# Performance work log

Hardware: AMD Instinct MI355X
Metric: run time of the kernel (lower is better)

The kernel has to match this reference:

```python
import jax, jax.numpy as jnp
import numpy as np

B, C, H, W = 4, 256, 64, 64
RED = 8
DQK = C // RED  # 32


def setup_inputs() -> dict:
    key = jax.random.key(0)
    ks = jax.random.split(key, 8)
    x = jax.random.normal(ks[0], (B, C, H, W), dtype=jnp.float32)
    # 1x1 conv weights == per-pixel linear maps: [out_ch, in_ch] + bias [out_ch]
    q_w = jax.random.normal(ks[1], (DQK, C), dtype=jnp.float32) * (1.0 / np.sqrt(C))
    q_b = jax.random.normal(ks[2], (DQK,), dtype=jnp.float32) * 0.01
    k_w = jax.random.normal(ks[3], (DQK, C), dtype=jnp.float32) * (1.0 / np.sqrt(C))
    k_b = jax.random.normal(ks[4], (DQK,), dtype=jnp.float32) * 0.01
    v_w = jax.random.normal(ks[5], (C, C), dtype=jnp.float32) * (1.0 / np.sqrt(C))
    v_b = jax.random.normal(ks[6], (C,), dtype=jnp.float32) * 0.01
    # gamma is init'd to 0 in torch; use a nonzero value so the attention path matters
    gamma = jax.random.normal(ks[7], (1,), dtype=jnp.float32) * 0.1
    return {"x": x, "q_w": q_w, "q_b": q_b, "k_w": k_w, "k_b": k_b,
            "v_w": v_w, "v_b": v_b, "gamma": gamma}


def reference(x, q_w, q_b, k_w, k_b, v_w, v_b, gamma):
    b, c, h, w = x.shape
    xf = x.reshape(b, c, h * w)  # [B, C, N]
    # 1x1 convs as channel matmuls
    q = jnp.einsum('dc,bcn->bdn', q_w, xf) + q_b[None, :, None]  # [B, DQK, N]
    k = jnp.einsum('dc,bcn->bdn', k_w, xf) + k_b[None, :, None]  # [B, DQK, N]
    v = jnp.einsum('oc,bcn->bon', v_w, xf) + v_b[None, :, None]  # [B, C, N]
    # attn[b, n, m] = softmax_m( q[:,n] . k[:,m] )  -- NO 1/sqrt(d) scale (faithful)
    scores = jnp.einsum('bdn,bdm->bnm', q, k)  # [B, N, N]
    attn = jax.nn.softmax(scores, axis=-1)
    # out = v @ attn^T : out[b, c, n] = sum_m v[b, c, m] * attn[b, n, m]
    out = jnp.einsum('bcm,bnm->bcn', v, attn).reshape(b, c, h, w)
    return gamma[0] * out + x
```

## Files before the change

kernel.cpp:

```cpp
#include <hip/hip_runtime.h>

#define NN 4096
#define CC 256
#define DQ 32

typedef __attribute__((ext_vector_type(8))) short short8;
typedef __attribute__((ext_vector_type(4))) float f32x4;

__device__ __forceinline__ unsigned short f32_to_bf16(float f) {
  unsigned int u = __float_as_uint(f);
  u += 0x7fffu + ((u >> 16) & 1u);
  return (unsigned short)(u >> 16);
}

__device__ __forceinline__ float exp2_hw(float f) {
  return __builtin_amdgcn_exp2f(f);
}

__device__ __forceinline__ unsigned cvt_pk_bf16(float lo, float hi) {
  unsigned r;
  asm("v_cvt_pk_bf16_f32 %0, %1, %2" : "=v"(r) : "v"(lo), "v"(hi));
  return r;
}

__device__ __forceinline__ void gld16(const void* g, void* l) {
  __builtin_amdgcn_global_load_lds(
      (__attribute__((address_space(1))) void*)(g),
      (__attribute__((address_space(3))) void*)(l), 16, 0, 0);
}

__global__ __launch_bounds__(256) void wconv_kernel(
    const float* qw, const float* kw, const float* vw,
    const float* qb, const float* kb, const float* vb,
    unsigned short* Wcat, float* bcat) {
  int id = blockIdx.x * 256 + threadIdx.x;
  if (id < 320 * 256) {
    int row = id >> 8;
    float v;
    if (row < 32) v = qw[id];
    else if (row < 64) v = kw[id - 32 * 256];
    else v = vw[id - 64 * 256];
    Wcat[id] = f32_to_bf16(v);
  }
  if (id < 320) {
    float v;
    if (id < 32) v = qb[id];
    else if (id < 64) v = kb[id - 32];
    else v = vb[id - 64];
    bcat[id] = v;
  }
}

__global__ __launch_bounds__(256) void proj_kernel(
    const float* x, const unsigned short* Wcat, const float* bcat,
    unsigned short* Qt, unsigned short* Kt, unsigned short* V) {
  int bid = blockIdx.x;
  int b = bid >> 6, nb = bid & 63;
  int tid = threadIdx.x, lane = tid & 63, w = tid >> 6;
  int l15 = lane & 15, h = lane >> 4;
  int n0 = nb * 64 + w * 16;

  __shared__ unsigned short xT[64][264];
  {
    const float* xb = x + ((size_t)b * CC) * NN + nb * 64;
    int c0 = tid >> 4, n4 = (tid & 15) * 4;
#pragma unroll
    for (int i = 0; i < 16; i++) {
      int c = c0 + i * 16;
      f32x4 v = *(const f32x4*)(xb + (size_t)c * NN + n4);
#pragma unroll
      for (int j = 0; j < 4; j++) xT[n4 + j][c] = f32_to_bf16(v[j]);
    }
  }
  __syncthreads();

  int nl = w * 16 + l15;
  short8 af[8];
#pragma unroll
  for (int ks = 0; ks < 8; ks++)
    af[ks] = *(const short8*)(&xT[nl][ks * 32 + h * 8]);

  f32x4 acc[20];
#pragma unroll
  for (int t = 0; t < 20; t++)
#pragma unroll
    for (int r = 0; r < 4; r++) acc[t][r] = 0.f;

#pragma unroll
  for (int ks = 0; ks < 8; ks++) {
#pragma unroll
    for (int dt = 0; dt < 20; dt++) {
      short8 bfr = *(const short8*)(Wcat + (size_t)(dt * 16 + l15) * CC + ks * 32 + h * 8);
      acc[dt] = __builtin_amdgcn_mfma_f32_16x16x32_bf16(af[ks], bfr, acc[dt], 0, 0, 0);
    }
  }

  unsigned short* Qtb = Qt + (size_t)b * NN * DQ;
  unsigned short* Ktb = Kt + (size_t)b * NN * DQ;
#pragma unroll
  for (int dt = 0; dt < 4; dt++) {
    float bias = bcat[dt * 16 + l15];
    float scale = dt < 2 ? 1.44269504f : 1.0f;
    unsigned short* dst = dt < 2 ? Qtb : Ktb;
    int dd = (dt & 1) * 16 + l15;
#pragma unroll
    for (int r = 0; r < 4; r++) {
      int n = n0 + h * 4 + r;
      dst[(size_t)n * DQ + dd] = f32_to_bf16((acc[dt][r] + bias) * scale);
    }
  }

  __shared__ unsigned short vbuf[CC][64];
  __syncthreads();
#pragma unroll
  for (int dt = 4; dt < 20; dt++) {
    float bias = bcat[dt * 16 + l15];
    int c = (dt - 4) * 16 + l15;
#pragma unroll
    for (int r = 0; r < 4; r++) {
      int nl2 = w * 16 + h * 4 + r;
      vbuf[c][nl2] = f32_to_bf16(acc[dt][r] + bias);
    }
  }
  __syncthreads();
  unsigned short* Vb = V + (size_t)b * CC * NN + nb * 64;
  for (int cc = 0; cc < 64; cc++) {
    int c = w * 64 + cc;
    Vb[(size_t)c * NN + lane] = vbuf[c][lane];
  }
}

__global__ __launch_bounds__(512) void attn_kernel(
    const unsigned short* Qt, const unsigned short* Kt, const unsigned short* V,
    const float* x, const float* gamma, float* out) {
  int bid = blockIdx.x;
  int b = (bid & 7) >> 1;
  int nb = (bid >> 3) * 2 + (bid & 1);
  int tid = threadIdx.x, lane = tid & 63, w = tid >> 6;
  int grp = w >> 2;
  int wq = w & 3;
  int wc = w & 3;
  int l15 = lane & 15, h = lane >> 4;
  int n0 = nb * 64 + wq * 16;

  const unsigned short* Qtb = Qt + (size_t)b * NN * DQ;
  const unsigned short* Ktb = Kt + (size_t)b * NN * DQ;
  const unsigned short* Vb  = V  + (size_t)b * CC * NN;

  __shared__ __align__(16) unsigned short vbuf[4][CC * 64];
  __shared__ __align__(16) unsigned short pbuf[8][16 * 64];
  __shared__ float sstat[8][16];

  short8 qf = *(const short8*)(Qtb + (size_t)(n0 + l15) * DQ + h * 8);

  f32x4 acc[16];
#pragma unroll
  for (int t = 0; t < 16; t++)
#pragma unroll
    for (int r = 0; r < 4; r++) acc[t][r] = 0.f;
  float rs = 0.f;

  f32x4 zero4;
#pragma unroll
  for (int r = 0; r < 4; r++) zero4[r] = 0.f;

  auto stageSS = [&](int t) {
#pragma unroll
    for (int ch = 0; ch < 2; ch++) {
      int ck = 2 * t + ch;
      int m0 = ck * 64;
      char* dst = (char*)&vbuf[ck & 3][0];
#pragma unroll
      for (int it = 0; it < 4; it++) {
        int idx = it * 512 + tid;
        int c = idx >> 3, sub = idx & 7;
        int moff = (sub ^ (c & 7)) * 8;
        gld16(Vb + (size_t)c * NN + m0 + moff, dst + idx * 16);
      }
    }
  };

#define KLOAD(T, KF) do { int ci_ = 2 * (T) + grp; \
  _Pragma("unroll") for (int s_ = 0; s_ < 4; s_++) \
    KF[s_] = *(const short8*)(Ktb + (size_t)(ci_ * 64 + s_ * 16 + l15) * DQ + h * 8); \
} while (0)

  short8 kA[4], kB[4];
  stageSS(0);
  KLOAD(0, kA);

#define SUPERSTEP(T, KF, KN) do { \
  __syncthreads();   \
  if ((T) + 1 < 32) stageSS((T) + 1); \
  f32x4 st[4]; \
  _Pragma("unroll") for (int s = 0; s < 4; s++) \
    st[s] = __builtin_amdgcn_mfma_f32_16x16x32_bf16(KF[s], qf, zero4, 0, 0, 0); \
  if ((T) + 1 < 32) KLOAD((T) + 1, KN); \
  float lsum = 0.f; \
  unsigned p32[8]; \
  _Pragma("unroll") for (int s = 0; s < 4; s++) { \
    float e0 = exp2_hw(st[s][0]); \
    float e1 = exp2_hw(st[s][1]); \
    float e2 = exp2_hw(st[s][2]); \
    float e3 = exp2_hw(st[s][3]); \
    lsum += (e0 + e1) + (e2 + e3); \
    p32[s * 2 + 0] = cvt_pk_bf16(e0, e1); \
    p32[s * 2 + 1] = cvt_pk_bf16(e2, e3); \
  } \
  rs += lsum; \
  { char* pb = (char*)&pbuf[w][0]; \
  _Pragma("unroll") for (int s = 0; s < 4; s++) { \
    int2 pv; pv.x = (int)p32[s * 2]; pv.y = (int)p32[s * 2 + 1]; \
    int inner = (s * 32 + h * 8) ^ ((l15 & 7) << 4); \
    *(int2*)(pb + l15 * 128 + inner) = pv; \
  } } \
   \
  asm volatile("s_waitcnt lgkmcnt(0)" ::: "memory"); \
  __builtin_amdgcn_s_barrier(); \
  asm volatile("" ::: "memory"); \
  { const char* vb2 = (const char*)&vbuf[(2 * (T) + grp) & 3][0]; \
  __builtin_amdgcn_s_setprio(1); \
  _Pragma("unroll") for (int p = 0; p < 2; p++) { \
    int pinner = (p * 64 + h * 16) ^ ((l15 & 7) << 4); \
    short8 pf0 = *(const short8*)((const char*)&pbuf[grp * 4 + 0][0] + l15 * 128 + pinner); \
    short8 pf1 = *(const short8*)((const char*)&pbuf[grp * 4 + 1][0] + l15 * 128 + pinner); \
    short8 pf2 = *(const short8*)((const char*)&pbuf[grp * 4 + 2][0] + l15 * 128 + pinner); \
    short8 pf3 = *(const short8*)((const char*)&pbuf[grp * 4 + 3][0] + l15 * 128 + pinner); \
    _Pragma("unroll") for (int ct = 0; ct < 4; ct++) { \
      int c = wc * 64 + ct * 16 + l15; \
      int sub = (p * 4 + h) ^ (c & 7); \
      short8 vf = *(const short8*)(vb2 + c * 128 + sub * 16); \
      acc[ct * 4 + 0] = __builtin_amdgcn_mfma_f32_16x16x32_bf16(vf, pf0, acc[ct * 4 + 0], 0, 0, 0); \
      acc[ct * 4 + 1] = __builtin_amdgcn_mfma_f32_16x16x32_bf16(vf, pf1, acc[ct * 4 + 1], 0, 0, 0); \
      acc[ct * 4 + 2] = __builtin_amdgcn_mfma_f32_16x16x32_bf16(vf, pf2, acc[ct * 4 + 2], 0, 0, 0); \
      acc[ct * 4 + 3] = __builtin_amdgcn_mfma_f32_16x16x32_bf16(vf, pf3, acc[ct * 4 + 3], 0, 0, 0); \
    } \
  } \
  __builtin_amdgcn_s_setprio(0); } \
} while (0)

  for (int t2 = 0; t2 < 16; t2++) {
    SUPERSTEP(2 * t2, kA, kB);
    SUPERSTEP(2 * t2 + 1, kB, kA);
  }
#undef SUPERSTEP
#undef KLOAD

  rs += __shfl_xor(rs, 16);
  rs += __shfl_xor(rs, 32);
  if (h == 0) sstat[w][l15] = rs;
  __syncthreads();

  float* sacc = (float*)&vbuf[0][0];
  if (grp == 1) {
#pragma unroll
    for (int ct = 0; ct < 4; ct++)
#pragma unroll
      for (int nt = 0; nt < 4; nt++)
        *(f32x4*)(sacc + ((wc * 16 + ct * 4 + nt) << 8) + lane * 4) = acc[ct * 4 + nt];
  }
  __syncthreads();

  if (grp == 0) {
    float g = gamma[0];
    float invv[4];
#pragma unroll
    for (int nt = 0; nt < 4; nt++)
      invv[nt] = 1.0f / (sstat[nt][l15] + sstat[4 + nt][l15]);
    const float* xb = x + (size_t)b * CC * NN;
    float* ob = out + (size_t)b * CC * NN;
#pragma unroll
    for (int ct = 0; ct < 4; ct++)
#pragma unroll
      for (int nt = 0; nt < 4; nt++) {
        f32x4 ap = *(const f32x4*)(sacc + ((wc * 16 + ct * 4 + nt) << 8) + lane * 4);
#pragma unroll
        for (int r = 0; r < 4; r++) {
          int c = wc * 64 + ct * 16 + h * 4 + r;
          size_t off = (size_t)c * NN + (size_t)nb * 64 + nt * 16 + l15;
          ob[off] = g * (acc[ct * 4 + nt][r] + ap[r]) * invv[nt] + xb[off];
        }
      }
  }
}

extern "C" void kernel_launch(void* const* d_in, const int* in_sizes, int n_in,
                              void* d_out, int out_size, void* d_ws, size_t ws_size,
                              hipStream_t stream) {
  (void)in_sizes; (void)n_in; (void)out_size; (void)ws_size;
  const float* x  = (const float*)d_in[0];
  const float* qw = (const float*)d_in[1];
  const float* qb = (const float*)d_in[2];
  const float* kw = (const float*)d_in[3];
  const float* kb = (const float*)d_in[4];
  const float* vw = (const float*)d_in[5];
  const float* vb = (const float*)d_in[6];
  const float* gamma = (const float*)d_in[7];
  float* out = (float*)d_out;

  char* ws = (char*)d_ws;
  unsigned short* Wcat = (unsigned short*)(ws);
  float*          bcat = (float*)(ws + 163840);
  unsigned short* Qt   = (unsigned short*)(ws + 165120);
  unsigned short* Kt   = (unsigned short*)(ws + 1213696);
  unsigned short* V    = (unsigned short*)(ws + 2262272);

  hipLaunchKernelGGL(wconv_kernel, dim3(320), dim3(256), 0, stream,
                     qw, kw, vw, qb, kb, vb, Wcat, bcat);
  hipLaunchKernelGGL(proj_kernel, dim3(256), dim3(256), 0, stream,
                     x, Wcat, bcat, Qt, Kt, V);
  hipLaunchKernelGGL(attn_kernel, dim3(256), dim3(512), 0, stream,
                     Qt, Kt, V, x, gamma, out);
}
```

Before: 105.0 us.

## Split attention over key halves with 1024-thread blocks and separate fuse kernel

The attention kernel now gives each block 128 query rows and half of the key range, using 16 waves per block. It writes bf16 partial outputs and row sums to workspace, and a new fuse kernel combines the two halves with the residual. The projection kernel also moves to 32-pixel tiles across 512 blocks, with vectorized V stores. The aim is more parallelism and wider query reuse of each staged V tile, at the cost of an extra launch, extra partial-buffer traffic and bf16 rounding of the partial sums.

```diff
diff --git a/kernel.cpp b/kernel.cpp
--- a/kernel.cpp
+++ b/kernel.cpp
@@ -11,6 +11,10 @@
   unsigned int u = __float_as_uint(f);
   u += 0x7fffu + ((u >> 16) & 1u);
   return (unsigned short)(u >> 16);
+}
+
+__device__ __forceinline__ float bf16_to_f32(unsigned short u) {
+  return __uint_as_float(((unsigned int)u) << 16);
 }
 
 __device__ __forceinline__ float exp2_hw(float f) {
@@ -55,18 +59,18 @@
     const float* x, const unsigned short* Wcat, const float* bcat,
     unsigned short* Qt, unsigned short* Kt, unsigned short* V) {
   int bid = blockIdx.x;
-  int b = bid >> 6, nb = bid & 63;
+  int b = bid >> 7, nb = bid & 127;
   int tid = threadIdx.x, lane = tid & 63, w = tid >> 6;
   int l15 = lane & 15, h = lane >> 4;
-  int n0 = nb * 64 + w * 16;
-
-  __shared__ unsigned short xT[64][264];
+
+  __shared__ unsigned short xT[32][272];
+  __shared__ unsigned short vbuf[CC][32];
   {
-    const float* xb = x + ((size_t)b * CC) * NN + nb * 64;
-    int c0 = tid >> 4, n4 = (tid & 15) * 4;
-#pragma unroll
-    for (int i = 0; i < 16; i++) {
-      int c = c0 + i * 16;
+    const float* xb = x + (size_t)b * CC * NN + nb * 32;
+    int c0 = tid >> 3, n4 = (tid & 7) * 4;
+#pragma unroll
+    for (int i = 0; i < 8; i++) {
+      int c = c0 + i * 32;
       f32x4 v = *(const f32x4*)(xb + (size_t)c * NN + n4);
 #pragma unroll
       for (int j = 0; j < 4; j++) xT[n4 + j][c] = f32_to_bf16(v[j]);
@@ -74,82 +78,76 @@
   }
   __syncthreads();
 
-  int nl = w * 16 + l15;
+  int ntile = w & 1, dt0 = (w >> 1) * 10;
   short8 af[8];
 #pragma unroll
   for (int ks = 0; ks < 8; ks++)
-    af[ks] = *(const short8*)(&xT[nl][ks * 32 + h * 8]);
-
-  f32x4 acc[20];
-#pragma unroll
-  for (int t = 0; t < 20; t++)
+    af[ks] = *(const short8*)(&xT[ntile * 16 + l15][ks * 32 + h * 8]);
+
+  f32x4 acc[10];
+#pragma unroll
+  for (int t = 0; t < 10; t++)
 #pragma unroll
     for (int r = 0; r < 4; r++) acc[t][r] = 0.f;
 
 #pragma unroll
   for (int ks = 0; ks < 8; ks++) {
 #pragma unroll
-    for (int dt = 0; dt < 20; dt++) {
+    for (int d = 0; d < 10; d++) {
+      int dt = dt0 + d;
       short8 bfr = *(const short8*)(Wcat + (size_t)(dt * 16 + l15) * CC + ks * 32 + h * 8);
-      acc[dt] = __builtin_amdgcn_mfma_f32_16x16x32_bf16(af[ks], bfr, acc[dt], 0, 0, 0);
+      acc[d] = __builtin_amdgcn_mfma_f32_16x16x32_bf16(af[ks], bfr, acc[d], 0, 0, 0);
     }
   }
 
   unsigned short* Qtb = Qt + (size_t)b * NN * DQ;
   unsigned short* Ktb = Kt + (size_t)b * NN * DQ;
 #pragma unroll
-  for (int dt = 0; dt < 4; dt++) {
+  for (int d = 0; d < 10; d++) {
+    int dt = dt0 + d;
     float bias = bcat[dt * 16 + l15];
-    float scale = dt < 2 ? 1.44269504f : 1.0f;
-    unsigned short* dst = dt < 2 ? Qtb : Ktb;
-    int dd = (dt & 1) * 16 + l15;
-#pragma unroll
-    for (int r = 0; r < 4; r++) {
-      int n = n0 + h * 4 + r;
-      dst[(size_t)n * DQ + dd] = f32_to_bf16((acc[dt][r] + bias) * scale);
-    }
-  }
-
-  __shared__ unsigned short vbuf[CC][64];
+    if (dt < 4) {
+      float scale = dt < 2 ? 1.44269504f : 1.0f;
+      unsigned short* dst = dt < 2 ? Qtb : Ktb;
+      int dd = (dt & 1) * 16 + l15;
+#pragma unroll
+      for (int r = 0; r < 4; r++) {
+        int n = nb * 32 + ntile * 16 + h * 4 + r;
+        dst[(size_t)n * DQ + dd] = f32_to_bf16((acc[d][r] + bias) * scale);
+      }
+    } else {
+      int c = (dt - 4) * 16 + l15;
+#pragma unroll
+      for (int r = 0; r < 4; r++)
+        vbuf[c][ntile * 16 + h * 4 + r] = f32_to_bf16(acc[d][r] + bias);
+    }
+  }
   __syncthreads();
-#pragma unroll
-  for (int dt = 4; dt < 20; dt++) {
-    float bias = bcat[dt * 16 + l15];
-    int c = (dt - 4) * 16 + l15;
-#pragma unroll
-    for (int r = 0; r < 4; r++) {
-      int nl2 = w * 16 + h * 4 + r;
-      vbuf[c][nl2] = f32_to_bf16(acc[dt][r] + bias);
-    }
-  }
-  __syncthreads();
-  unsigned short* Vb = V + (size_t)b * CC * NN + nb * 64;
-  for (int cc = 0; cc < 64; cc++) {
-    int c = w * 64 + cc;
-    Vb[(size_t)c * NN + lane] = vbuf[c][lane];
-  }
-}
-
-__global__ __launch_bounds__(512) void attn_kernel(
+  unsigned short* Vb = V + (size_t)b * CC * NN + nb * 32;
+  int c = tid;
+#pragma unroll
+  for (int k = 0; k < 4; k++)
+    *(f32x4*)(Vb + (size_t)c * NN + k * 8) = *(const f32x4*)(&vbuf[c][k * 8]);
+}
+
+__global__ __launch_bounds__(1024) void attn_kernel(
     const unsigned short* Qt, const unsigned short* Kt, const unsigned short* V,
-    const float* x, const float* gamma, float* out) {
+    unsigned short* Apart, float* rspart) {
   int bid = blockIdx.x;
-  int b = (bid & 7) >> 1;
-  int nb = (bid >> 3) * 2 + (bid & 1);
+  int b  = (bid & 7) >> 1;
+  int mh = bid & 1;
+  int nb = bid >> 3;
   int tid = threadIdx.x, lane = tid & 63, w = tid >> 6;
-  int grp = w >> 2;
-  int wq = w & 3;
-  int wc = w & 3;
+  int grp = w >> 3, wq = w & 7, wc = w & 3, ntb = (w >> 2) & 1;
   int l15 = lane & 15, h = lane >> 4;
-  int n0 = nb * 64 + wq * 16;
+  int n0 = nb * 128 + wq * 16;
 
   const unsigned short* Qtb = Qt + (size_t)b * NN * DQ;
   const unsigned short* Ktb = Kt + (size_t)b * NN * DQ;
   const unsigned short* Vb  = V  + (size_t)b * CC * NN;
 
-  __shared__ __align__(16) unsigned short vbuf[4][CC * 64];
-  __shared__ __align__(16) unsigned short pbuf[8][16 * 64];
-  __shared__ float sstat[8][16];
+  __shared__ __align__(16) unsigned short lds[81920];
+  char* ldsb = (char*)lds;
 
   short8 qf = *(const short8*)(Qtb + (size_t)(n0 + l15) * DQ + h * 8);
 
@@ -167,12 +165,12 @@
   auto stageSS = [&](int t) {
 #pragma unroll
     for (int ch = 0; ch < 2; ch++) {
-      int ck = 2 * t + ch;
+      int ck = mh * 32 + 2 * t + ch;
+      char* dst = ldsb + (ck & 3) * 32768;
       int m0 = ck * 64;
-      char* dst = (char*)&vbuf[ck & 3][0];
-#pragma unroll
-      for (int it = 0; it < 4; it++) {
-        int idx = it * 512 + tid;
+#pragma unroll
+      for (int it = 0; it < 2; it++) {
+        int idx = it * 1024 + tid;
         int c = idx >> 3, sub = idx & 7;
         int moff = (sub ^ (c & 7)) * 8;
         gld16(Vb + (size_t)c * NN + m0 + moff, dst + idx * 16);
@@ -180,7 +178,7 @@
     }
   };
 
-#define KLOAD(T, KF) do { int ci_ = 2 * (T) + grp; \
+#define KLOAD(T, KF) do { int ci_ = mh * 32 + 2 * (T) + grp; \
   _Pragma("unroll") for (int s_ = 0; s_ < 4; s_++) \
     KF[s_] = *(const short8*)(Ktb + (size_t)(ci_ * 64 + s_ * 16 + l15) * DQ + h * 8); \
 } while (0)
@@ -191,11 +189,11 @@
 
 #define SUPERSTEP(T, KF, KN) do { \
   __syncthreads();   \
-  if ((T) + 1 < 32) stageSS((T) + 1); \
+  if ((T) + 1 < 16) stageSS((T) + 1); \
   f32x4 st[4]; \
   _Pragma("unroll") for (int s = 0; s < 4; s++) \
     st[s] = __builtin_amdgcn_mfma_f32_16x16x32_bf16(KF[s], qf, zero4, 0, 0, 0); \
-  if ((T) + 1 < 32) KLOAD((T) + 1, KN); \
+  if ((T) + 1 < 16) KLOAD((T) + 1, KN); \
   float lsum = 0.f; \
   unsigned p32[8]; \
   _Pragma("unroll") for (int s = 0; s < 4; s++) { \
@@ -208,24 +206,24 @@
     p32[s * 2 + 1] = cvt_pk_bf16(e2, e3); \
   } \
   rs += lsum; \
-  { char* pb = (char*)&pbuf[w][0]; \
+  { char* pb = ldsb + 131072 + w * 2048; \
   _Pragma("unroll") for (int s = 0; s < 4; s++) { \
     int2 pv; pv.x = (int)p32[s * 2]; pv.y = (int)p32[s * 2 + 1]; \
     int inner = (s * 32 + h * 8) ^ ((l15 & 7) << 4); \
     *(int2*)(pb + l15 * 128 + inner) = pv; \
   } } \
-   \
   asm volatile("s_waitcnt lgkmcnt(0)" ::: "memory"); \
   __builtin_amdgcn_s_barrier(); \
   asm volatile("" ::: "memory"); \
-  { const char* vb2 = (const char*)&vbuf[(2 * (T) + grp) & 3][0]; \
+  { const char* vb2 = ldsb + ((2 * (T) + grp) & 3) * 32768; \
+  const char* pbase = ldsb + 131072 + (grp * 8 + ntb * 4) * 2048; \
   __builtin_amdgcn_s_setprio(1); \
   _Pragma("unroll") for (int p = 0; p < 2; p++) { \
     int pinner = (p * 64 + h * 16) ^ ((l15 & 7) << 4); \
-    short8 pf0 = *(const short8*)((const char*)&pbuf[grp * 4 + 0][0] + l15 * 128 + pinner); \
-    short8 pf1 = *(const short8*)((const char*)&pbuf[grp * 4 + 1][0] + l15 * 128 + pinner); \
-    short8 pf2 = *(const short8*)((const char*)&pbuf[grp * 4 + 2][0] + l15 * 128 + pinner); \
-    short8 pf3 = *(const short8*)((const char*)&pbuf[grp * 4 + 3][0] + l15 * 128 + pinner); \
+    short8 pf0 = *(const short8*)(pbase + 0 * 2048 + l15 * 128 + pinner); \
+    short8 pf1 = *(const short8*)(pbase + 1 * 2048 + l15 * 128 + pinner); \
+    short8 pf2 = *(const short8*)(pbase + 2 * 2048 + l15 * 128 + pinner); \
+    short8 pf3 = *(const short8*)(pbase + 3 * 2048 + l15 * 128 + pinner); \
     _Pragma("unroll") for (int ct = 0; ct < 4; ct++) { \
       int c = wc * 64 + ct * 16 + l15; \
       int sub = (p * 4 + h) ^ (c & 7); \
@@ -239,7 +237,7 @@
   __builtin_amdgcn_s_setprio(0); } \
 } while (0)
 
-  for (int t2 = 0; t2 < 16; t2++) {
+  for (int t2 = 0; t2 < 8; t2++) {
     SUPERSTEP(2 * t2, kA, kB);
     SUPERSTEP(2 * t2 + 1, kB, kA);
   }
@@ -248,40 +246,89 @@
 
   rs += __shfl_xor(rs, 16);
   rs += __shfl_xor(rs, 32);
-  if (h == 0) sstat[w][l15] = rs;
+  if (h == 0)
+    rspart[(size_t)(b * 4 + mh * 2 + grp) * NN + nb * 128 + wq * 16 + l15] = rs;
+
   __syncthreads();
-
-  float* sacc = (float*)&vbuf[0][0];
-  if (grp == 1) {
+  char* pregion = ldsb + 131072;
+  for (int r = 0; r < 4; r++) {
+    if (grp == 1) {
+#pragma unroll
+      for (int i = 0; i < 4; i++)
+        *(f32x4*)(pregion + (w - 8) * 4096 + i * 1024 + lane * 16) = acc[r * 4 + i];
+    }
+    __syncthreads();
+    if (grp == 0) {
+#pragma unroll
+      for (int i = 0; i < 4; i++) {
+        f32x4 p = *(const f32x4*)(pregion + w * 4096 + i * 1024 + lane * 16);
+#pragma unroll
+        for (int q = 0; q < 4; q++) acc[r * 4 + i][q] += p[q];
+      }
+    }
+    __syncthreads();
+  }
+
+  if (grp == 0) {
 #pragma unroll
     for (int ct = 0; ct < 4; ct++)
 #pragma unroll
-      for (int nt = 0; nt < 4; nt++)
-        *(f32x4*)(sacc + ((wc * 16 + ct * 4 + nt) << 8) + lane * 4) = acc[ct * 4 + nt];
-  }
-  __syncthreads();
-
-  if (grp == 0) {
-    float g = gamma[0];
-    float invv[4];
-#pragma unroll
-    for (int nt = 0; nt < 4; nt++)
-      invv[nt] = 1.0f / (sstat[nt][l15] + sstat[4 + nt][l15]);
-    const float* xb = x + (size_t)b * CC * NN;
-    float* ob = out + (size_t)b * CC * NN;
-#pragma unroll
-    for (int ct = 0; ct < 4; ct++)
-#pragma unroll
-      for (int nt = 0; nt < 4; nt++) {
-        f32x4 ap = *(const f32x4*)(sacc + ((wc * 16 + ct * 4 + nt) << 8) + lane * 4);
+      for (int i = 0; i < 4; i++)
 #pragma unroll
         for (int r = 0; r < 4; r++) {
           int c = wc * 64 + ct * 16 + h * 4 + r;
-          size_t off = (size_t)c * NN + (size_t)nb * 64 + nt * 16 + l15;
-          ob[off] = g * (acc[ct * 4 + nt][r] + ap[r]) * invv[nt] + xb[off];
+          int n = (ntb * 4 + i) * 16 + l15;
+          lds[c * 128 + n] = f32_to_bf16(acc[ct * 4 + i][r]);
         }
-      }
-  }
+  }
+  __syncthreads();
+  {
+    unsigned short* Adst = Apart + (size_t)(b * 2 + mh) * CC * NN + nb * 128;
+    int c = tid >> 2, seg = tid & 3;
+    const f32x4* src = (const f32x4*)(ldsb + c * 256 + seg * 64);
+#pragma unroll
+    for (int k = 0; k < 4; k++)
+      *(f32x4*)(Adst + (size_t)c * NN + seg * 32 + k * 8) = src[k];
+  }
+}
+
+__global__ __launch_bounds__(256) void fuse_kernel(
+    const unsigned short* Apart, const float* rspart, const float* x,
+    const float* gamma, float* out) {
+  int bid = blockIdx.x;
+  int b = bid >> 9, c = (bid >> 1) & 255, half = bid & 1;
+  int n0 = half * 2048 + threadIdx.x * 8;
+
+  short8 a0 = *(const short8*)(Apart + ((size_t)(b * 2 + 0) * CC + c) * NN + n0);
+  short8 a1 = *(const short8*)(Apart + ((size_t)(b * 2 + 1) * CC + c) * NN + n0);
+
+  const float* rp = rspart + (size_t)b * 4 * NN + n0;
+  f32x4 rlo, rhi;
+#pragma unroll
+  for (int q = 0; q < 4; q++) { rlo[q] = 0.f; rhi[q] = 0.f; }
+#pragma unroll
+  for (int p = 0; p < 4; p++) {
+    f32x4 ra = *(const f32x4*)(rp + (size_t)p * NN);
+    f32x4 rb = *(const f32x4*)(rp + (size_t)p * NN + 4);
+#pragma unroll
+    for (int q = 0; q < 4; q++) { rlo[q] += ra[q]; rhi[q] += rb[q]; }
+  }
+
+  const float* xp = x + ((size_t)b * CC + c) * NN + n0;
+  f32x4 x0 = *(const f32x4*)(xp), x1 = *(const f32x4*)(xp + 4);
+  float g = gamma[0];
+
+  f32x4 o0, o1;
+#pragma unroll
+  for (int q = 0; q < 4; q++) {
+    float a = bf16_to_f32((unsigned short)a0[q]) + bf16_to_f32((unsigned short)a1[q]);
+    o0[q] = g * a / rlo[q] + x0[q];
+    float a2 = bf16_to_f32((unsigned short)a0[q + 4]) + bf16_to_f32((unsigned short)a1[q + 4]);
+    o1[q] = g * a2 / rhi[q] + x1[q];
+  }
+  float* op = out + ((size_t)b * CC + c) * NN + n0;
+  *(f32x4*)op = o0;
+  *(f32x4*)(op + 4) = o1;
 }
 
 extern "C" void kernel_launch(void* const* d_in, const int* in_sizes, int n_in,
@@ -299,16 +346,20 @@
   float* out = (float*)d_out;
 
   char* ws = (char*)d_ws;
-  unsigned short* Wcat = (unsigned short*)(ws);
-  float*          bcat = (float*)(ws + 163840);
-  unsigned short* Qt   = (unsigned short*)(ws + 165120);
-  unsigned short* Kt   = (unsigned short*)(ws + 1213696);
-  unsigned short* V    = (unsigned short*)(ws + 2262272);
+  unsigned short* Wcat  = (unsigned short*)(ws);
+  float*          bcat  = (float*)(ws + 163840);
+  unsigned short* Qt    = (unsigned short*)(ws + 165120);
+  unsigned short* Kt    = (unsigned short*)(ws + 1213696);
+  unsigned short* V     = (unsigned short*)(ws + 2262272);
+  unsigned short* Apart = (unsigned short*)(ws + 10650880);
+  float*          rsprt = (float*)(ws + 27428096);
 
   hipLaunchKernelGGL(wconv_kernel, dim3(320), dim3(256), 0, stream,
                      qw, kw, vw, qb, kb, vb, Wcat, bcat);
-  hipLaunchKernelGGL(proj_kernel, dim3(256), dim3(256), 0, stream,
+  hipLaunchKernelGGL(proj_kernel, dim3(512), dim3(256), 0, stream,
                      x, Wcat, bcat, Qt, Kt, V);
-  hipLaunchKernelGGL(attn_kernel, dim3(256), dim3(512), 0, stream,
-                     Qt, Kt, V, x, gamma, out);
-}
+  hipLaunchKernelGGL(attn_kernel, dim3(256), dim3(1024), 0, stream,
+                     Qt, Kt, V, Apart, rsprt);
+  hipLaunchKernelGGL(fuse_kernel, dim3(2048), dim3(256), 0, stream,
+                     Apart, rsprt, x, gamma, out);
+}
```

Result: slower. 200.1 us (+90.5%).
